# Kernel optimization log

Measured on AMD Instinct MI355X. Metric: run time of the kernel, lower is better.

Reference implementation:

```python
import jax, jax.numpy as jnp
import numpy as np

D_MODEL = 1024
HEADS = 16
HEAD_DIM = D_MODEL // HEADS


def setup_inputs() -> dict:
    key = jax.random.key(0)
    k1, k2 = jax.random.split(key)
    x = jax.random.normal(k1, (2, 2048, D_MODEL), dtype=jnp.float32)
    # nn.Linear(d_model, 3*d_model, bias=False): weight shape [3*d_model, d_model]
    W_qkv = jax.random.normal(k2, (3 * D_MODEL, D_MODEL), dtype=jnp.float32) * (D_MODEL ** -0.5)
    return {"x": x, "W_qkv": W_qkv}


def reference(x, W_qkv):
    b, t, c = x.shape
    qkv = jnp.einsum('btc,fc->btf', x, W_qkv)  # [b, t, 3c]
    q, k, v = jnp.split(qkv, 3, axis=-1)
    # [b, heads, t, head_dim]
    q = q.reshape(b, t, HEADS, HEAD_DIM).transpose(0, 2, 1, 3)
    k = k.reshape(b, t, HEADS, HEAD_DIM).transpose(0, 2, 1, 3)
    v = v.reshape(b, t, HEADS, HEAD_DIM).transpose(0, 2, 1, 3)
    scores = jnp.einsum('bhqd,bhkd->bhqk', q, k) * (HEAD_DIM ** -0.5)
    causal = jnp.tril(jnp.ones((t, t), dtype=bool))  # [t, t]
    scores = jnp.where(causal[None, None, :, :], scores, -jnp.inf)
    weights = jax.nn.softmax(scores, axis=-1)
    out = jnp.einsum('bhqk,bhkd->bhqd', weights, v)
    return out.transpose(0, 2, 1, 3).reshape(b, t, c)
```

## Files before the change

### kernel.cpp

```cpp
#include <hip/hip_runtime.h>
#include <hip/hip_bf16.h>
#include <stdint.h>

#define D_MODEL 1024
#define TOKENS  2048
#define HEADS   16
#define HDIM    64
#define NQKV    3072
#define MROWS   4096
#define SCALE   0.18033688011112042f

typedef __attribute__((ext_vector_type(4)))  float f32x4;
typedef __attribute__((ext_vector_type(16))) float f32x16;
typedef __attribute__((ext_vector_type(8)))  short bf16x8;

__device__ __forceinline__ unsigned short f2bf(float f) {
  union { float f; unsigned u; } v; v.f = f;
  unsigned u = v.u + 0x7FFFu + ((v.u >> 16) & 1u);
  return (unsigned short)(u >> 16);
}
__device__ __forceinline__ float bf2f(unsigned short b) {
  union { unsigned u; float f; } v; v.u = ((unsigned)b) << 16;
  return v.f;
}
__device__ __forceinline__ unsigned cvt_pk_bf16(float lo, float hi) {
  unsigned r;
  asm("v_cvt_pk_bf16_f32 %0, %1, %2" : "=v"(r) : "v"(lo), "v"(hi));
  return r;
}
__device__ __forceinline__ float xchg32(float v) {
  return __shfl_xor(v, 32);
}
__device__ __forceinline__ bf16x8 pfrag8(const float* g) {
  union { uint4 u; bf16x8 v; } r;
  r.u.x = cvt_pk_bf16(g[0], g[1]);
  r.u.y = cvt_pk_bf16(g[2], g[3]);
  r.u.z = cvt_pk_bf16(g[4], g[5]);
  r.u.w = cvt_pk_bf16(g[6], g[7]);
  return r.v;
}
__device__ __forceinline__ float max32t(const f32x16& a, const f32x16& b) {
  float t[16];
#pragma unroll
  for (int r = 0; r < 16; ++r) t[r] = fmaxf(a[r], b[r]);
#pragma unroll
  for (int s = 8; s > 0; s >>= 1)
#pragma unroll
    for (int r = 0; r < s; ++r) t[r] = fmaxf(t[r], t[r + s]);
  return t[0];
}
__device__ __forceinline__ float sum32t(const float* a, const float* b) {
  float t[16];
#pragma unroll
  for (int r = 0; r < 16; ++r) t[r] = a[r] + b[r];
#pragma unroll
  for (int s = 8; s > 0; s >>= 1)
#pragma unroll
    for (int r = 0; r < s; ++r) t[r] = t[r] + t[r + s];
  return t[0];
}

#define GLOAD16(g, l)                                                          \
  __builtin_amdgcn_global_load_lds(                                            \
      (const __attribute__((address_space(1))) unsigned int*)(g),              \
      (__attribute__((address_space(3))) unsigned int*)(l), 16, 0, 0)

__global__ __launch_bounds__(256) void cvt_bf16(const float* __restrict__ X,
                                                const float* __restrict__ W,
                                                unsigned short* __restrict__ Xb,
                                                unsigned short* __restrict__ Wb) {
  const size_t NX = (size_t)MROWS * D_MODEL;
  size_t i = ((size_t)blockIdx.x * 256 + threadIdx.x) * 8;
  const float* src; unsigned short* dst; size_t off;
  if (i < NX) { src = X; dst = Xb; off = i; }
  else        { src = W; dst = Wb; off = i - NX; }
  float4 a = ((const float4*)(src + off))[0];
  float4 b = ((const float4*)(src + off))[1];
  union { unsigned short s[8]; uint4 v; } u;
  u.s[0] = f2bf(a.x); u.s[1] = f2bf(a.y); u.s[2] = f2bf(a.z); u.s[3] = f2bf(a.w);
  u.s[4] = f2bf(b.x); u.s[5] = f2bf(b.y); u.s[6] = f2bf(b.z); u.s[7] = f2bf(b.w);
  *(uint4*)(dst + off) = u.v;
}

__global__ __launch_bounds__(512, 1) void gemm8(const unsigned short* __restrict__ A,
                                                const unsigned short* __restrict__ B,
                                                unsigned short* __restrict__ C) {
  __shared__ unsigned short sA[2][2][128][64];
  __shared__ unsigned short sB[2][2][128][64];

  const int tid  = threadIdx.x;
  const int lane = tid & 63;
  const int wave = tid >> 6;
  const int wr   = wave >> 2;
  const int wc   = wave & 3;
  const int l15  = lane & 15;
  const int lg   = lane >> 4;

  const int bm = blockIdx.x;
  const int bn = blockIdx.y;

  f32x4 acc[8][4];
#pragma unroll
  for (int i = 0; i < 8; ++i)
#pragma unroll
    for (int j = 0; j < 4; ++j)
#pragma unroll
      for (int r = 0; r < 4; ++r) acc[i][j][r] = 0.f;

  const int srow = tid >> 3;
  const int scb  = (tid & 7) * 16;
  const int ssce = (scb ^ ((srow & 7) << 4)) >> 1;

  const unsigned short* Ag = A + (size_t)(bm * 256) * D_MODEL;
  const unsigned short* Bg = B + (size_t)(bn * 256) * D_MODEL;

#define STG_A(buf, hf, t)                                                      \
  { GLOAD16(Ag + (size_t)((hf) * 128 + srow) * D_MODEL + (t) * 64 + ssce,      \
            (char*)&sA[buf][hf][0][0] + srow * 128 + scb);                     \
    GLOAD16(Ag + (size_t)((hf) * 128 + 64 + srow) * D_MODEL + (t) * 64 + ssce, \
            (char*)&sA[buf][hf][0][0] + 8192 + srow * 128 + scb); }
#define STG_B(buf, hf, t)                                                      \
  { GLOAD16(Bg + (size_t)((hf) * 128 + srow) * D_MODEL + (t) * 64 + ssce,      \
            (char*)&sB[buf][hf][0][0] + srow * 128 + scb);                     \
    GLOAD16(Bg + (size_t)((hf) * 128 + 64 + srow) * D_MODEL + (t) * 64 + ssce, \
            (char*)&sB[buf][hf][0][0] + 8192 + srow * 128 + scb); }

  const char* aBse[2] = { (const char*)&sA[0][wr][0][0], (const char*)&sA[1][wr][0][0] };
  const char* bBse[2] = { (const char*)&sB[0][wc >> 1][0][0], (const char*)&sB[1][wc >> 1][0][0] };
  const int swzl = (l15 & 7) << 4;
  const int cbs0 = (lg * 16) ^ swzl;
  const int cbs1 = (64 + lg * 16) ^ swzl;
  const int arow = l15 * 128;
  const int brow = ((wc & 1) * 64 + l15) * 128;

  bf16x8 aF[4][2];

#define DO_PHASE(qm, qn, buf, LD_A, STAGE_STMT, DO_VM)                         \
  {                                                                            \
    if (LD_A) {                                                                \
      _Pragma("unroll")                                                        \
      for (int i = 0; i < 4; ++i) {                                            \
        aF[i][0] = *(const bf16x8*)(aBse[buf] + ((qm)*4 + i) * 2048 + arow + cbs0); \
        aF[i][1] = *(const bf16x8*)(aBse[buf] + ((qm)*4 + i) * 2048 + arow + cbs1); \
      }                                                                        \
    }                                                                          \
    bf16x8 b_[2][2];                                                           \
    _Pragma("unroll")                                                          \
    for (int n = 0; n < 2; ++n) {                                              \
      b_[n][0] = *(const bf16x8*)(bBse[buf] + ((qn)*2 + n) * 2048 + brow + cbs0); \
      b_[n][1] = *(const bf16x8*)(bBse[buf] + ((qn)*2 + n) * 2048 + brow + cbs1); \
    }                                                                          \
    STAGE_STMT;                                                                \
    if (DO_VM) asm volatile("s_waitcnt vmcnt(2)" ::: "memory");                \
    __builtin_amdgcn_s_barrier();                                              \
    asm volatile("s_waitcnt lgkmcnt(0)" ::: "memory");                         \
    __builtin_amdgcn_sched_barrier(0);                                         \
    __builtin_amdgcn_s_setprio(1);                                             \
    _Pragma("unroll")                                                          \
    for (int ks = 0; ks < 2; ++ks)                                             \
      _Pragma("unroll")                                                        \
      for (int i = 0; i < 4; ++i)                                              \
        _Pragma("unroll")                                                      \
        for (int n = 0; n < 2; ++n)                                            \
          acc[(qm)*4 + i][(qn)*2 + n] = __builtin_amdgcn_mfma_f32_16x16x32_bf16( \
              aF[i][ks], b_[n][ks], acc[(qm)*4 + i][(qn)*2 + n], 0, 0, 0);     \
    __builtin_amdgcn_s_setprio(0);                                             \
    __builtin_amdgcn_s_barrier();                                              \
  }

  STG_A(0, 0, 0);
  STG_B(0, 0, 0);
  STG_A(0, 1, 0);
  STG_B(0, 1, 0);
  STG_B(1, 0, 1);
  asm volatile("s_waitcnt vmcnt(2)" ::: "memory");
  __builtin_amdgcn_s_barrier();

#pragma unroll 1
  for (int j = 0; j < 8; ++j) {
    const int t1 = 2 * j + 1;
    const int t2 = 2 * j + 2;
    const int t3 = 2 * j + 3;
    DO_PHASE(0, 0, 0, 1, { STG_A(1, 0, t1); }, 0);
    DO_PHASE(0, 1, 0, 0, { STG_A(1, 1, t1); }, 0);
    DO_PHASE(1, 0, 0, 1, { STG_B(1, 1, t1); }, 0);
    DO_PHASE(1, 1, 0, 0, { if (t2 < 16) STG_B(0, 0, t2); }, 1);
    DO_PHASE(0, 0, 1, 1, { if (t2 < 16) STG_A(0, 0, t2); }, 0);
    DO_PHASE(0, 1, 1, 0, { if (t2 < 16) STG_A(0, 1, t2); }, 0);
    DO_PHASE(1, 0, 1, 1, { if (t2 < 16) STG_B(0, 1, t2); }, 0);
    DO_PHASE(1, 1, 1, 0, { if (t3 < 16) STG_B(1, 0, t3); }, 1);
  }

  const int orow0 = bm * 256 + wr * 128 + lg * 4;
  const int ocol0 = bn * 256 + wc * 64 + l15;
#pragma unroll
  for (int mi = 0; mi < 8; ++mi)
#pragma unroll
    for (int ni = 0; ni < 4; ++ni)
#pragma unroll
      for (int r = 0; r < 4; ++r)
        C[(size_t)(orow0 + mi * 16 + r) * NQKV + ocol0 + ni * 16] = f2bf(acc[mi][ni][r]);
#undef STG_A
#undef STG_B
#undef DO_PHASE
}

__global__ __launch_bounds__(256) void qkv_gemm(const float* __restrict__ X,
                                                const float* __restrict__ W,
                                                unsigned short* __restrict__ QKV) {
  __shared__ unsigned short sA[128 * 32];
  __shared__ unsigned short sB[128 * 32];
  const int tid  = threadIdx.x;
  const int lane = tid & 63;
  const int wave = tid >> 6;
  const int wr = wave >> 1, wc = wave & 1;
  const int row0 = blockIdx.x * 128;
  const int col0 = blockIdx.y * 128;

  f32x4 acc[4][4];
#pragma unroll
  for (int i = 0; i < 4; ++i)
#pragma unroll
    for (int j = 0; j < 4; ++j)
#pragma unroll
      for (int r = 0; r < 4; ++r) acc[i][j][r] = 0.f;

  const int srow = tid >> 1;
  const int scol = (tid & 1) * 16;
  union U16 { unsigned short s[8]; uint4 v; };

#pragma unroll 1
  for (int k0 = 0; k0 < D_MODEL; k0 += 32) {
    {
      const float* ga = X + (size_t)(row0 + srow) * D_MODEL + k0 + scol;
      const float* gb = W + (size_t)(col0 + srow) * D_MODEL + k0 + scol;
      float va[16], vb[16];
#pragma unroll
      for (int i = 0; i < 4; ++i) {
        float4 t = ((const float4*)ga)[i];
        va[4*i+0] = t.x; va[4*i+1] = t.y; va[4*i+2] = t.z; va[4*i+3] = t.w;
        float4 u = ((const float4*)gb)[i];
        vb[4*i+0] = u.x; vb[4*i+1] = u.y; vb[4*i+2] = u.z; vb[4*i+3] = u.w;
      }
      U16 ua0, ua1, ub0, ub1;
#pragma unroll
      for (int e = 0; e < 8; ++e) {
        ua0.s[e] = f2bf(va[e]);   ua1.s[e] = f2bf(va[8 + e]);
        ub0.s[e] = f2bf(vb[e]);   ub1.s[e] = f2bf(vb[8 + e]);
      }
      *(uint4*)&sA[srow * 32 + scol + 0] = ua0.v;
      *(uint4*)&sA[srow * 32 + scol + 8] = ua1.v;
      *(uint4*)&sB[srow * 32 + scol + 0] = ub0.v;
      *(uint4*)&sB[srow * 32 + scol + 8] = ub1.v;
    }
    __syncthreads();

    const int lrow = lane & 15;
    const int lk   = (lane >> 4) * 8;
    bf16x8 av[4], bv[4];
#pragma unroll
    for (int i = 0; i < 4; ++i)
      av[i] = *(const bf16x8*)&sA[(wr * 64 + i * 16 + lrow) * 32 + lk];
#pragma unroll
    for (int j = 0; j < 4; ++j)
      bv[j] = *(const bf16x8*)&sB[(wc * 64 + j * 16 + lrow) * 32 + lk];
#pragma unroll
    for (int i = 0; i < 4; ++i)
#pragma unroll
      for (int j = 0; j < 4; ++j)
        acc[i][j] = __builtin_amdgcn_mfma_f32_16x16x32_bf16(av[i], bv[j], acc[i][j], 0, 0, 0);
    __syncthreads();
  }

  const int orow = row0 + wr * 64 + (lane >> 4) * 4;
  const int ocol = col0 + wc * 64 + (lane & 15);
#pragma unroll
  for (int i = 0; i < 4; ++i)
#pragma unroll
    for (int j = 0; j < 4; ++j)
#pragma unroll
      for (int r = 0; r < 4; ++r)
        QKV[(size_t)(orow + i * 16 + r) * NQKV + ocol + j * 16] = f2bf(acc[i][j][r]);
}

__global__ __launch_bounds__(512, 2) void attn13(const unsigned short* __restrict__ QKV,
                                                 float* __restrict__ Out) {
  __shared__ unsigned short sK [2][2][64 * 64];
  __shared__ unsigned short sVt[2][2][64 * 64];

  const int tid  = threadIdx.x;
  const int lane = tid & 63;
  const int wave = tid >> 6;
  const int wq   = wave & 3;
  const int ws   = wave >> 2;
  const int l31  = lane & 31;
  const int hi   = lane >> 5;

  const int x = blockIdx.x;
  int bh, u;
  if (x < 256) { bh = x & 31; u = x >> 5; }
  else         { const int x2 = x - 256; bh = x2 & 31; u = 15 - (x2 >> 5); }

  const int b = bh >> 4, h = bh & 15;
  const int q0w  = u * 128 + wq * 32;
  const int qcol = q0w + l31;

  const unsigned short* Qbase = QKV + (size_t)(b * TOKENS) * NQKV + h * HDIM;
  const unsigned short* Kbase = Qbase + D_MODEL;
  const unsigned short* Vbase = Kbase + D_MODEL;

  bf16x8 qf[4];
  {
    const unsigned short* qrow = Qbase + (size_t)qcol * NQKV + hi * 8;
    union { unsigned short us[8]; bf16x8 v; ushort4 q[2]; } t;
#pragma unroll
    for (int dk = 0; dk < 4; ++dk) {
      t.q[0] = ((const ushort4*)(qrow + dk * 16))[0];
      t.q[1] = ((const ushort4*)(qrow + dk * 16))[1];
#pragma unroll
      for (int e = 0; e < 8; ++e) t.us[e] = f2bf(bf2f(t.us[e]) * SCALE);
      qf[dk] = t.v;
    }
  }

  f32x16 o0a, o0b, o1a, o1b;
#pragma unroll
  for (int r = 0; r < 16; ++r) { o0a[r] = 0.f; o0b[r] = 0.f; o1a[r] = 0.f; o1b[r] = 0.f; }
  float m = -1e30f, ll = 0.f;

  const int kd    = tid * 16;
  const int krow  = kd >> 7;
  const int kgrow = (krow & 51) | ((krow & 4) << 1) | ((krow & 8) >> 1);
  const int kcb   = (kd & 127) ^ ((krow & 7) << 4);
  const int vk0   = (tid & 31) * 2;
  const int vd0   = (tid >> 5) * 4;
  union VU { ushort4 v; unsigned short us[4]; };
  VU va0, va1, vb0, vb1;

#define KGLOAD(kt, buf, s)                                                     \
  GLOAD16(Kbase + (size_t)((kt) * 64 + kgrow) * NQKV + (kcb >> 1),             \
          (char*)&sK[buf][s][0] + kd);

#define VLOADP(pp)                                                             \
  {                                                                            \
    const unsigned short* vsA = Vbase + (size_t)((2*(pp)) * 64 + vk0) * NQKV + vd0;   \
    va0.v = *(const ushort4*)(vsA);                                            \
    va1.v = *(const ushort4*)(vsA + NQKV);                                     \
    const unsigned short* vsB = Vbase + (size_t)((2*(pp)+1) * 64 + vk0) * NQKV + vd0; \
    vb0.v = *(const ushort4*)(vsB);                                            \
    vb1.v = *(const ushort4*)(vsB + NQKV);                                     \
  }

#define VWRITEP(buf)                                                           \
  {                                                                            \
    char* dA = (char*)&sVt[buf][0][0];                                         \
    char* dB = (char*)&sVt[buf][1][0];                                         \
    _Pragma("unroll")                                                          \
    for (int e = 0; e < 4; ++e) {                                              \
      const int dim = vd0 + e;                                                 \
      const int o2 = (dim * 128 + vk0 * 2) ^ ((dim & 7) << 4);                 \
      *(unsigned*)(dA + o2) = (unsigned)va0.us[e] | ((unsigned)va1.us[e] << 16); \
      *(unsigned*)(dB + o2) = (unsigned)vb0.us[e] | ((unsigned)vb1.us[e] << 16); \
    }                                                                          \
  }

#define QKT(cK, rowbase, st)                                                   \
  {                                                                            \
    _Pragma("unroll")                                                          \
    for (int dk = 0; dk < 4; ++dk) {                                           \
      const int row = (rowbase);                                               \
      bf16x8 kf = *(const bf16x8*)((cK) + ((row * 128 + hi * 16 + dk * 32) ^ ((row & 7) << 4))); \
      st = __builtin_amdgcn_mfma_f32_32x32x16_bf16(kf, qf[dk], st, 0, 0, 0);   \
    }                                                                          \
  }

#define PV4(cV, bpX, bpY, koff)                                                \
  {                                                                            \
    const int r0 = l31, r1 = l31 + 32;                                         \
    bf16x8 vf;                                                                 \
    vf = *(const bf16x8*)((cV) + ((r0 * 128 + hi * 16 + (koff)) ^ ((r0 & 7) << 4)));      \
    o0a = __builtin_amdgcn_mfma_f32_32x32x16_bf16(vf, bpX, o0a, 0, 0, 0);      \
    vf = *(const bf16x8*)((cV) + ((r1 * 128 + hi * 16 + (koff)) ^ ((r1 & 7) << 4)));      \
    o1a = __builtin_amdgcn_mfma_f32_32x32x16_bf16(vf, bpX, o1a, 0, 0, 0);      \
    vf = *(const bf16x8*)((cV) + ((r0 * 128 + hi * 16 + (koff) + 32) ^ ((r0 & 7) << 4))); \
    o0b = __builtin_amdgcn_mfma_f32_32x32x16_bf16(vf, bpY, o0b, 0, 0, 0);      \
    vf = *(const bf16x8*)((cV) + ((r1 * 128 + hi * 16 + (koff) + 32) ^ ((r1 & 7) << 4))); \
    o1b = __builtin_amdgcn_mfma_f32_32x32x16_bf16(vf, bpY, o1b, 0, 0, 0);      \
  }

#define MUPDATE(mx)                                                            \
  {                                                                            \
    if (!__all((mx) - m <= 8.f)) {                                             \
      float mw = fmaxf((mx), xchg32(mx));                                      \
      const float mnew = fmaxf(m, mw);                                         \
      const float corr = exp2f(m - mnew);                                      \
      m = mnew;                                                                \
      ll *= corr;                                                              \
      _Pragma("unroll")                                                        \
      for (int r = 0; r < 16; ++r) {                                           \
        o0a[r] *= corr; o0b[r] *= corr; o1a[r] *= corr; o1b[r] *= corr;        \
      }                                                                        \
    }                                                                          \
  }

  KGLOAD(0, 0, 0);
  KGLOAD(1, 0, 1);
  VLOADP(0);
  VWRITEP(0);
  __syncthreads();

#pragma unroll 1
  for (int p = 0; p < u; ++p) {
    const int cur = p & 1;
    KGLOAD(2 * (p + 1),     cur ^ 1, 0);
    KGLOAD(2 * (p + 1) + 1, cur ^ 1, 1);
    VLOADP(p + 1);

    {
      const char* cK = (const char*)&sK[cur][ws][0];
      const char* cV = (const char*)&sVt[cur][ws][0];
      f32x16 st0, st1;
#pragma unroll
      for (int r = 0; r < 16; ++r) { st0[r] = 0.f; st1[r] = 0.f; }
      QKT(cK, l31,      st0);
      QKT(cK, l31 + 32, st1);
      float mx = max32t(st0, st1);
      MUPDATE(mx);
      float p0[16], p1[16];
#pragma unroll
      for (int r = 0; r < 16; ++r) { p0[r] = exp2f(st0[r] - m); p1[r] = exp2f(st1[r] - m); }
      ll += sum32t(p0, p1);
      bf16x8 f0 = pfrag8(&p0[0]), f1 = pfrag8(&p0[8]);
      bf16x8 f2 = pfrag8(&p1[0]), f3 = pfrag8(&p1[8]);
      PV4(cV, f0, f1, 0);
      PV4(cV, f2, f3, 64);
    }

    VWRITEP(cur ^ 1);
    __syncthreads();
  }

  {
    const int cur = u & 1;
    const bool skip = (ws == 1) && (wq < 2);
    if (!skip) {
      const bool diag  = (ws == 0) ? (wq < 2) : true;
      const bool do_hi = diag ? ((wq & 1) == 1) : true;
      const int kbase = u * 128 + ws * 64;
      const char* cK = (const char*)&sK[cur][ws][0];
      const char* cV = (const char*)&sVt[cur][ws][0];

      f32x16 st0, st1;
#pragma unroll
      for (int r = 0; r < 16; ++r) { st0[r] = 0.f; st1[r] = 0.f; }
      QKT(cK, l31, st0);
      if (do_hi) QKT(cK, l31 + 32, st1);

      if (diag) {
#pragma unroll
        for (int r = 0; r < 16; ++r) {
          const int key0 = kbase + (r & 7) + ((r & 8) << 1) + 8 * hi;
          if (key0 > qcol) st0[r] = -1e30f;
          if (do_hi && key0 + 32 > qcol) st1[r] = -1e30f;
        }
      }

      float mx = do_hi ? max32t(st0, st1) : max32t(st0, st0);
      MUPDATE(mx);

      float p0[16], p1[16];
#pragma unroll
      for (int r = 0; r < 16; ++r) p0[r] = exp2f(st0[r] - m);
      if (do_hi) {
#pragma unroll
        for (int r = 0; r < 16; ++r) p1[r] = exp2f(st1[r] - m);
        ll += sum32t(p0, p1);
      } else {
        float z[16];
#pragma unroll
        for (int r = 0; r < 16; ++r) z[r] = 0.f;
        ll += sum32t(p0, z);
      }

      bf16x8 c0 = pfrag8(&p0[0]), c1 = pfrag8(&p0[8]);
      PV4(cV, c0, c1, 0);
      if (do_hi) {
        bf16x8 c2 = pfrag8(&p1[0]), c3 = pfrag8(&p1[8]);
        PV4(cV, c2, c3, 64);
      }
    }
  }

  __syncthreads();
  const float lfull = ll + xchg32(ll);
#pragma unroll
  for (int r = 0; r < 16; ++r) { o0a[r] += o0b[r]; o1a[r] += o1b[r]; }

  float* slot = (wq < 2)
      ? ((float*)&sK [0][0][0] + (size_t)(( wq      * 64 + lane) * 35))
      : ((float*)&sVt[0][0][0] + (size_t)(((wq - 2) * 64 + lane) * 35));

  if (ws == 1) {
    slot[0] = m;
    slot[1] = lfull;
#pragma unroll
    for (int r = 0; r < 16; ++r) slot[2 + r]  = o0a[r];
#pragma unroll
    for (int r = 0; r < 16; ++r) slot[18 + r] = o1a[r];
  }
  __syncthreads();
  if (ws == 0) {
    const float mB = slot[0];
    const float lB = slot[1];
    const float M  = fmaxf(m, mB);
    const float wA = exp2f(m - M);
    const float wB = exp2f(mB - M);
    const float inv = 1.f / (lfull * wA + lB * wB);
    float* orow = Out + (size_t)(b * TOKENS + qcol) * D_MODEL + h * HDIM;
#pragma unroll
    for (int g = 0; g < 4; ++g) {
      float4 w0, w1;
      w0.x = (o0a[4*g+0] * wA + slot[2 + 4*g+0] * wB) * inv;
      w0.y = (o0a[4*g+1] * wA + slot[2 + 4*g+1] * wB) * inv;
      w0.z = (o0a[4*g+2] * wA + slot[2 + 4*g+2] * wB) * inv;
      w0.w = (o0a[4*g+3] * wA + slot[2 + 4*g+3] * wB) * inv;
      w1.x = (o1a[4*g+0] * wA + slot[18 + 4*g+0] * wB) * inv;
      w1.y = (o1a[4*g+1] * wA + slot[18 + 4*g+1] * wB) * inv;
      w1.z = (o1a[4*g+2] * wA + slot[18 + 4*g+2] * wB) * inv;
      w1.w = (o1a[4*g+3] * wA + slot[18 + 4*g+3] * wB) * inv;
      *(float4*)(orow + 8 * g + 4 * hi)      = w0;
      *(float4*)(orow + 8 * g + 4 * hi + 32) = w1;
    }
  }
#undef KGLOAD
#undef VLOADP
#undef VWRITEP
#undef QKT
#undef PV4
#undef MUPDATE
}

extern "C" void kernel_launch(void* const* d_in, const int* in_sizes, int n_in,
                              void* d_out, int out_size, void* d_ws, size_t ws_size,
                              hipStream_t stream) {
  const float* X = (const float*)d_in[0];
  const float* W = (const float*)d_in[1];
  float* Out = (float*)d_out;
  unsigned short* QKV = (unsigned short*)d_ws;

  const size_t QKV_E = (size_t)MROWS * NQKV;
  const size_t XB_E  = (size_t)MROWS * D_MODEL;
  const size_t WB_E  = (size_t)NQKV * D_MODEL;
  const size_t need_bf16 = (QKV_E + XB_E + WB_E) * 2;

  if (ws_size >= need_bf16) {
    unsigned short* Xb = QKV + QKV_E;
    unsigned short* Wb = Xb + XB_E;
    cvt_bf16<<<(XB_E + WB_E) / (256 * 8), 256, 0, stream>>>(X, W, Xb, Wb);
    gemm8<<<dim3(MROWS / 256, NQKV / 256), 512, 0, stream>>>(Xb, Wb, QKV);
  } else {
    qkv_gemm<<<dim3(MROWS / 128, NQKV / 128), 256, 0, stream>>>(X, W, QKV);
  }

  attn13<<<512, 512, 0, stream>>>(QKV, Out);
}
```

Before: 94.30 us.

## Split attention into 64-query blocks with 4 waves and single-buffered V

The attention kernel now uses 1024 blocks of 256 threads, each covering 64 queries instead of 128. Blocks are ordered longest-first, replacing the previous paired-block balancing. V is held in a single LDS buffer with one wider transposed write per thread, and an extra barrier per iteration guards that buffer. The aim is smaller, better-balanced work units and less LDS per block so more blocks fit per CU. In exchange the loop takes two syncs per iteration and K/V tiles are reloaded by more blocks.

```diff
diff --git a/kernel.cpp b/kernel.cpp
--- a/kernel.cpp
+++ b/kernel.cpp
@@ -283,27 +283,28 @@
         QKV[(size_t)(orow + i * 16 + r) * NQKV + ocol + j * 16] = f2bf(acc[i][j][r]);
 }
 
-__global__ __launch_bounds__(512, 2) void attn13(const unsigned short* __restrict__ QKV,
+__global__ __launch_bounds__(256, 3) void attn14(const unsigned short* __restrict__ QKV,
                                                  float* __restrict__ Out) {
-  __shared__ unsigned short sK [2][2][64 * 64];
-  __shared__ unsigned short sVt[2][2][64 * 64];
+  __shared__ unsigned short sK[2][2][64 * 64];
+  __shared__ unsigned short sV[2][64 * 64];
 
   const int tid  = threadIdx.x;
   const int lane = tid & 63;
   const int wave = tid >> 6;
-  const int wq   = wave & 3;
-  const int ws   = wave >> 2;
+  const int wq   = wave & 1;
+  const int ws   = wave >> 1;
   const int l31  = lane & 31;
   const int hi   = lane >> 5;
 
-  const int x = blockIdx.x;
-  int bh, u;
-  if (x < 256) { bh = x & 31; u = x >> 5; }
-  else         { const int x2 = x - 256; bh = x2 & 31; u = 15 - (x2 >> 5); }
-
+  const int x  = blockIdx.x;
+  const int u  = 31 - (x >> 5);
+  const int bh = x & 31;
   const int b = bh >> 4, h = bh & 15;
-  const int q0w  = u * 128 + wq * 32;
+
+  const int q0w  = u * 64 + wq * 32;
   const int qcol = q0w + l31;
+  const int np   = u >> 1;
+  const int dsub = u & 1;
 
   const unsigned short* Qbase = QKV + (size_t)(b * TOKENS) * NQKV + h * HDIM;
   const unsigned short* Kbase = Qbase + D_MODEL;
@@ -328,39 +329,53 @@
   for (int r = 0; r < 16; ++r) { o0a[r] = 0.f; o0b[r] = 0.f; o1a[r] = 0.f; o1b[r] = 0.f; }
   float m = -1e30f, ll = 0.f;
 
-  const int kd    = tid * 16;
-  const int krow  = kd >> 7;
-  const int kgrow = (krow & 51) | ((krow & 4) << 1) | ((krow & 8) >> 1);
-  const int kcb   = (kd & 127) ^ ((krow & 7) << 4);
-  const int vk0   = (tid & 31) * 2;
-  const int vd0   = (tid >> 5) * 4;
-  union VU { ushort4 v; unsigned short us[4]; };
-  VU va0, va1, vb0, vb1;
+  const int vk0 = (tid & 15) * 4;
+  const int vd0 = (tid >> 4) * 4;
+  ushort4 va0, va1, va2, va3, vb0, vb1, vb2, vb3;
+  const int lane16 = lane * 16;
 
 #define KGLOAD(kt, buf, s)                                                     \
-  GLOAD16(Kbase + (size_t)((kt) * 64 + kgrow) * NQKV + (kcb >> 1),             \
-          (char*)&sK[buf][s][0] + kd);
+  {                                                                            \
+    _Pragma("unroll")                                                          \
+    for (int g = 0; g < 2; ++g) {                                              \
+      const int base = g * 4096 + wave * 1024;                                 \
+      const int d = base + lane16;                                             \
+      const int row = d >> 7;                                                  \
+      const int grow = (row & 51) | ((row & 4) << 1) | ((row & 8) >> 1);       \
+      const int cb = (d & 127) ^ ((row & 7) << 4);                             \
+      GLOAD16(Kbase + (size_t)((kt) * 64 + grow) * NQKV + (cb >> 1),           \
+              (char*)&sK[buf][s][0] + base + lane16);                          \
+    }                                                                          \
+  }
 
 #define VLOADP(pp)                                                             \
   {                                                                            \
     const unsigned short* vsA = Vbase + (size_t)((2*(pp)) * 64 + vk0) * NQKV + vd0;   \
-    va0.v = *(const ushort4*)(vsA);                                            \
-    va1.v = *(const ushort4*)(vsA + NQKV);                                     \
+    va0 = *(const ushort4*)(vsA);                                              \
+    va1 = *(const ushort4*)(vsA + NQKV);                                       \
+    va2 = *(const ushort4*)(vsA + 2 * NQKV);                                   \
+    va3 = *(const ushort4*)(vsA + 3 * NQKV);                                   \
     const unsigned short* vsB = Vbase + (size_t)((2*(pp)+1) * 64 + vk0) * NQKV + vd0; \
-    vb0.v = *(const ushort4*)(vsB);                                            \
-    vb1.v = *(const ushort4*)(vsB + NQKV);                                     \
-  }
-
-#define VWRITEP(buf)                                                           \
-  {                                                                            \
-    char* dA = (char*)&sVt[buf][0][0];                                         \
-    char* dB = (char*)&sVt[buf][1][0];                                         \
+    vb0 = *(const ushort4*)(vsB);                                              \
+    vb1 = *(const ushort4*)(vsB + NQKV);                                       \
+    vb2 = *(const ushort4*)(vsB + 2 * NQKV);                                   \
+    vb3 = *(const ushort4*)(vsB + 3 * NQKV);                                   \
+  }
+
+#define VWRITE1(s, t0, t1, t2, t3)                                             \
+  {                                                                            \
+    ushort4 c0, c1, c2, c3;                                                    \
+    c0.x = t0.x; c0.y = t1.x; c0.z = t2.x; c0.w = t3.x;                        \
+    c1.x = t0.y; c1.y = t1.y; c1.z = t2.y; c1.w = t3.y;                        \
+    c2.x = t0.z; c2.y = t1.z; c2.z = t2.z; c2.w = t3.z;                        \
+    c3.x = t0.w; c3.y = t1.w; c3.z = t2.w; c3.w = t3.w;                        \
+    char* dV = (char*)&sV[s][0];                                               \
     _Pragma("unroll")                                                          \
     for (int e = 0; e < 4; ++e) {                                              \
       const int dim = vd0 + e;                                                 \
       const int o2 = (dim * 128 + vk0 * 2) ^ ((dim & 7) << 4);                 \
-      *(unsigned*)(dA + o2) = (unsigned)va0.us[e] | ((unsigned)va1.us[e] << 16); \
-      *(unsigned*)(dB + o2) = (unsigned)vb0.us[e] | ((unsigned)vb1.us[e] << 16); \
+      ushort4 cc = (e == 0) ? c0 : (e == 1) ? c1 : (e == 2) ? c2 : c3;         \
+      *(ushort4*)(dV + o2) = cc;                                               \
     }                                                                          \
   }
 
@@ -406,11 +421,12 @@
   KGLOAD(0, 0, 0);
   KGLOAD(1, 0, 1);
   VLOADP(0);
-  VWRITEP(0);
+  VWRITE1(0, va0, va1, va2, va3);
+  VWRITE1(1, vb0, vb1, vb2, vb3);
   __syncthreads();
 
 #pragma unroll 1
-  for (int p = 0; p < u; ++p) {
+  for (int p = 0; p < np; ++p) {
     const int cur = p & 1;
     KGLOAD(2 * (p + 1),     cur ^ 1, 0);
     KGLOAD(2 * (p + 1) + 1, cur ^ 1, 1);
@@ -418,7 +434,7 @@
 
     {
       const char* cK = (const char*)&sK[cur][ws][0];
-      const char* cV = (const char*)&sVt[cur][ws][0];
+      const char* cV = (const char*)&sV[ws][0];
       f32x16 st0, st1;
 #pragma unroll
       for (int r = 0; r < 16; ++r) { st0[r] = 0.f; st1[r] = 0.f; }
@@ -436,19 +452,21 @@
       PV4(cV, f2, f3, 64);
     }
 
-    VWRITEP(cur ^ 1);
     __syncthreads();
+    VWRITE1(0, va0, va1, va2, va3);
+    VWRITE1(1, vb0, vb1, vb2, vb3);
+    __syncthreads();
   }
 
   {
-    const int cur = u & 1;
-    const bool skip = (ws == 1) && (wq < 2);
+    const int cur = np & 1;
+    const bool skip = (ws == 1) && (dsub == 0);
     if (!skip) {
-      const bool diag  = (ws == 0) ? (wq < 2) : true;
-      const bool do_hi = diag ? ((wq & 1) == 1) : true;
-      const int kbase = u * 128 + ws * 64;
+      const bool isdiag = (ws == dsub);
+      const bool do_hi  = isdiag ? (wq == 1) : true;
+      const int kbase = np * 128 + ws * 64;
       const char* cK = (const char*)&sK[cur][ws][0];
-      const char* cV = (const char*)&sVt[cur][ws][0];
+      const char* cV = (const char*)&sV[ws][0];
 
       f32x16 st0, st1;
 #pragma unroll
@@ -456,12 +474,12 @@
       QKT(cK, l31, st0);
       if (do_hi) QKT(cK, l31 + 32, st1);
 
-      if (diag) {
+      if (isdiag) {
 #pragma unroll
         for (int r = 0; r < 16; ++r) {
           const int key0 = kbase + (r & 7) + ((r & 8) << 1) + 8 * hi;
-          if (key0 > qcol) st0[r] = -1e30f;
-          if (do_hi && key0 + 32 > qcol) st1[r] = -1e30f;
+          if (wq == 0) { if (key0 > qcol) st0[r] = -1e30f; }
+          else         { if (key0 + 32 > qcol) st1[r] = -1e30f; }
         }
       }
 
@@ -496,9 +514,7 @@
 #pragma unroll
   for (int r = 0; r < 16; ++r) { o0a[r] += o0b[r]; o1a[r] += o1b[r]; }
 
-  float* slot = (wq < 2)
-      ? ((float*)&sK [0][0][0] + (size_t)(( wq      * 64 + lane) * 35))
-      : ((float*)&sVt[0][0][0] + (size_t)(((wq - 2) * 64 + lane) * 35));
+  float* slot = (float*)&sK[0][0][0] + (size_t)((wq * 64 + lane) * 34);
 
   if (ws == 1) {
     slot[0] = m;
@@ -534,7 +550,7 @@
   }
 #undef KGLOAD
 #undef VLOADP
-#undef VWRITEP
+#undef VWRITE1
 #undef QKT
 #undef PV4
 #undef MUPDATE
@@ -562,5 +578,5 @@
     qkv_gemm<<<dim3(MROWS / 128, NQKV / 128), 256, 0, stream>>>(X, W, QKV);
   }
 
-  attn13<<<512, 512, 0, stream>>>(QKV, Out);
-}
+  attn14<<<1024, 256, 0, stream>>>(QKV, Out);
+}
```

New measurement: 105.9 us. 12.3% more time.

## Triple-buffer K tiles in attention and prefetch two iterations ahead

Applied to the files above, without the earlier changes.

Grows the K shared-memory buffer from two to three stages so the async K loads are issued two iterations ahead, while V stays double-buffered. The full __syncthreads is replaced by explicit vmcnt/lgkmcnt waits plus a raw s_barrier, so loads still in flight for the next K tile are not drained each iteration. The goal is to hide global-load latency better. In exchange it uses more LDS per block, which may threaten two blocks per CU, and depends on hand-counted vmcnt values being correct.

```diff
diff --git a/kernel.cpp b/kernel.cpp
--- a/kernel.cpp
+++ b/kernel.cpp
@@ -283,9 +283,9 @@
         QKV[(size_t)(orow + i * 16 + r) * NQKV + ocol + j * 16] = f2bf(acc[i][j][r]);
 }
 
-__global__ __launch_bounds__(512, 2) void attn13(const unsigned short* __restrict__ QKV,
+__global__ __launch_bounds__(512, 2) void attn15(const unsigned short* __restrict__ QKV,
                                                  float* __restrict__ Out) {
-  __shared__ unsigned short sK [2][2][64 * 64];
+  __shared__ unsigned short sK [3][2][64 * 64];
   __shared__ unsigned short sVt[2][2][64 * 64];
 
   const int tid  = threadIdx.x;
@@ -405,20 +405,30 @@
 
   KGLOAD(0, 0, 0);
   KGLOAD(1, 0, 1);
+  if (u >= 1) {
+    KGLOAD(2, 1, 0);
+    KGLOAD(3, 1, 1);
+  }
   VLOADP(0);
   VWRITEP(0);
   __syncthreads();
 
 #pragma unroll 1
   for (int p = 0; p < u; ++p) {
-    const int cur = p & 1;
-    KGLOAD(2 * (p + 1),     cur ^ 1, 0);
-    KGLOAD(2 * (p + 1) + 1, cur ^ 1, 1);
+    const int kcur = p % 3;
+    const int vcur = p & 1;
+    const bool more2 = (p + 2 <= u);
+
     VLOADP(p + 1);
+    if (more2) {
+      const int kb2 = (p + 2) % 3;
+      KGLOAD(2 * (p + 2),     kb2, 0);
+      KGLOAD(2 * (p + 2) + 1, kb2, 1);
+    }
 
     {
-      const char* cK = (const char*)&sK[cur][ws][0];
-      const char* cV = (const char*)&sVt[cur][ws][0];
+      const char* cK = (const char*)&sK[kcur][ws][0];
+      const char* cV = (const char*)&sVt[vcur][ws][0];
       f32x16 st0, st1;
 #pragma unroll
       for (int r = 0; r < 16; ++r) { st0[r] = 0.f; st1[r] = 0.f; }
@@ -436,19 +446,23 @@
       PV4(cV, f2, f3, 64);
     }
 
-    VWRITEP(cur ^ 1);
-    __syncthreads();
+    if (more2) asm volatile("s_waitcnt vmcnt(2)" ::: "memory");
+    else       asm volatile("s_waitcnt vmcnt(0)" ::: "memory");
+    VWRITEP(vcur ^ 1);
+    asm volatile("s_waitcnt lgkmcnt(0)" ::: "memory");
+    __builtin_amdgcn_s_barrier();
   }
 
   {
-    const int cur = u & 1;
+    const int kcur = u % 3;
+    const int vcur = u & 1;
     const bool skip = (ws == 1) && (wq < 2);
     if (!skip) {
       const bool diag  = (ws == 0) ? (wq < 2) : true;
       const bool do_hi = diag ? ((wq & 1) == 1) : true;
       const int kbase = u * 128 + ws * 64;
-      const char* cK = (const char*)&sK[cur][ws][0];
-      const char* cV = (const char*)&sVt[cur][ws][0];
+      const char* cK = (const char*)&sK[kcur][ws][0];
+      const char* cV = (const char*)&sVt[vcur][ws][0];
 
       f32x16 st0, st1;
 #pragma unroll
@@ -562,5 +576,5 @@
     qkv_gemm<<<dim3(MROWS / 128, NQKV / 128), 256, 0, stream>>>(X, W, QKV);
   }
 
-  attn13<<<512, 512, 0, stream>>>(QKV, Out);
-}
+  attn15<<<512, 512, 0, stream>>>(QKV, Out);
+}
```

New measurement: 97.10 us. 1.03x slower.
